# Kernel optimization log

Hardware: AMD Instinct MI355X
Metric: run time of the kernel (lower is better)

Reference implementation:

```python
import jax, jax.numpy as jnp
import numpy as np
from jax import lax

FPS_NUM, K = 2048, 32


def fps_subsample(x, n):
    # x: [B, N, 3] -> [B, n, 3]; farthest point sampling, deterministic start at index 0
    B, N, _ = x.shape
    d0 = jnp.sum((x - x[:, :1]) ** 2, axis=-1)  # [B, N] dist to point 0

    def step(dists, _):
        nxt = jnp.argmax(dists, axis=1)                       # [B]
        p = x[jnp.arange(B), nxt]                             # [B, 3]
        dists = jnp.minimum(dists, jnp.sum((x - p[:, None]) ** 2, axis=-1))
        return dists, nxt

    _, idxs = lax.scan(step, d0, None, length=n - 1)          # [n-1, B]
    idxs = jnp.concatenate([jnp.zeros((1, B), jnp.int32), idxs.astype(jnp.int32)], axis=0).T  # [B, n]
    return x[jnp.arange(B)[:, None], idxs]                    # [B, n, 3]


def knn_idx(x, k):
    # x: [B, C, N] -> [B, N, k] indices of k nearest neighbors in feature space
    xx = jnp.sum(x * x, axis=1)                               # [B, N]
    inner = jnp.einsum('bcn,bcm->bnm', x, x)
    neg_dist = 2.0 * inner - xx[:, :, None] - xx[:, None, :]  # -||xi-xj||^2
    return lax.top_k(neg_dist, k)[1]


def get_graph_feature(x, k):
    # DGCNN edge features: x [B, C, N] -> [B, 2C, N, k]
    B, C, N = x.shape
    idx = knn_idx(x, k)                                       # [B, N, k]
    xt = jnp.transpose(x, (0, 2, 1))                          # [B, N, C]
    nbr = xt[jnp.arange(B)[:, None, None], idx]               # [B, N, k, C]
    ctr = jnp.broadcast_to(xt[:, :, None], nbr.shape)
    feat = jnp.concatenate([nbr - ctr, ctr], axis=-1)         # [B, N, k, 2C]
    return jnp.transpose(feat, (0, 3, 1, 2))


def attention(xq, xk, pos, Wq, bq, Wk, bk, Wv, bv, Wp, bp):
    # positional attention over k neighbors: xq/xk [B, Cin, N, k], pos [B, 3, N] -> [B, dim, N]
    q = jnp.einsum('bcnk,dc->bdnk', xq, Wq) + bq[:, None, None]
    kk = jnp.einsum('bcnk,dc->bdnk', xk, Wk) + bk[:, None, None]
    v = jnp.einsum('bcnk,dc->bdnk', xk, Wv) + bv[:, None, None]
    p = jnp.einsum('bcn,dc->bdn', pos, Wp) + bp[:, None]      # [B, dim, N]
    dim = Wq.shape[0]
    logits = jnp.einsum('bdnk,bdnk->bnk', q, kk) / jnp.sqrt(jnp.float32(dim))
    attn = jax.nn.softmax(logits, axis=-1)                    # [B, N, k]
    return jnp.einsum('bnk,bdnk->bdn', attn, v + p[:, :, :, None])


def _layer_params(key, cin, dim):
    ks = jax.random.split(key, 4)
    s = 1.0 / np.sqrt(cin)
    return (jax.random.normal(ks[0], (dim, cin), jnp.float32) * s,
            jnp.zeros((dim,), jnp.float32),
            jax.random.normal(ks[1], (dim, cin), jnp.float32) * s,
            jnp.zeros((dim,), jnp.float32),
            jax.random.normal(ks[2], (dim, cin), jnp.float32) * s,
            jnp.zeros((dim,), jnp.float32),
            jax.random.normal(ks[3], (dim, 3), jnp.float32) * (1.0 / np.sqrt(3.0)),
            jnp.zeros((dim,), jnp.float32))


def setup_inputs() -> dict:
    key = jax.random.key(0)
    kx, k1, k2, k3 = jax.random.split(key, 4)
    x = jax.random.normal(kx, (8, 16384, 3), jnp.float32)
    out = {'x': x}
    for name, kk_, cin, dim in (('t1', k1, 6, 64), ('t2', k2, 128, 64), ('t3', k3, 128, 128)):
        Wq, bq, Wk, bk, Wv, bv, Wp, bp = _layer_params(kk_, cin, dim)
        out.update({f'{name}_Wq': Wq, f'{name}_bq': bq, f'{name}_Wk': Wk, f'{name}_bk': bk,
                    f'{name}_Wv': Wv, f'{name}_bv': bv, f'{name}_Wp': Wp, f'{name}_bp': bp})
    return out


def reference(x, t1_Wq, t1_bq, t1_Wk, t1_bk, t1_Wv, t1_bv, t1_Wp, t1_bp,
              t2_Wq, t2_bq, t2_Wk, t2_bk, t2_Wv, t2_bv, t2_Wp, t2_bp,
              t3_Wq, t3_bq, t3_Wk, t3_bk, t3_Wv, t3_bv, t3_Wp, t3_bp):
    partial = jnp.transpose(fps_subsample(x, FPS_NUM), (0, 2, 1))       # [B, 3, n]
    g = get_graph_feature(partial, K)                                    # [B, 6, n, k]
    x1 = attention(g, g, partial, t1_Wq, t1_bq, t1_Wk, t1_bk, t1_Wv, t1_bv, t1_Wp, t1_bp)  # [B, 64, n]
    g = get_graph_feature(x1, K)                                         # [B, 128, n, k]
    x2 = attention(g, g, partial, t2_Wq, t2_bq, t2_Wk, t2_bk, t2_Wv, t2_bv, t2_Wp, t2_bp)  # [B, 64, n]
    g = get_graph_feature(x2, K)                                         # [B, 128, n, k]
    x3 = attention(g, g, partial, t3_Wq, t3_bq, t3_Wk, t3_bk, t3_Wv, t3_bv, t3_Wp, t3_bp)  # [B, 128, n]
    feats = jnp.concatenate([x1, x2, x3], axis=1)                        # [B, 256, n]
    return jnp.concatenate([jnp.max(feats, axis=-1), jnp.mean(feats, axis=-1)], axis=1)    # [B, 512]
```

## Files before the change

### kernel.cpp

```cpp
#include <hip/hip_runtime.h>
#include <math.h>

#define NB 8
#define NIN 16384
#define NP 2048
#define KNN 32
#define TOTPTS (NB * NP)

#define NEG_INF (-__builtin_inff())

__device__ __forceinline__ float2 pk_add(float2 a, float2 b) {
  float2 d;
  asm("v_pk_add_f32 %0, %1, %2" : "=v"(d) : "v"(a), "v"(b));
  return d;
}
__device__ __forceinline__ float2 pk_mul(float2 a, float2 b) {
  float2 d;
  asm("v_pk_mul_f32 %0, %1, %2" : "=v"(d) : "v"(a), "v"(b));
  return d;
}

#define DPP_F(old, v, C, RM) \
  __int_as_float(__builtin_amdgcn_update_dpp(__float_as_int(old), __float_as_int(v), C, RM, 0xf, false))
#define DPP_I(old, v, C, RM) \
  __builtin_amdgcn_update_dpp(old, v, C, RM, 0xf, false)

__device__ __forceinline__ float wave_max_f(float v) {
  v = fmaxf(v, DPP_F(NEG_INF, v, 0x111, 0xf));
  v = fmaxf(v, DPP_F(NEG_INF, v, 0x112, 0xf));
  v = fmaxf(v, DPP_F(NEG_INF, v, 0x114, 0xf));
  v = fmaxf(v, DPP_F(NEG_INF, v, 0x118, 0xf));
  v = fmaxf(v, DPP_F(NEG_INF, v, 0x142, 0xa));
  v = fmaxf(v, DPP_F(NEG_INF, v, 0x143, 0xc));
  return v;
}
__device__ __forceinline__ int wave_min_i(int v) {
  v = min(v, DPP_I(0x7fffffff, v, 0x111, 0xf));
  v = min(v, DPP_I(0x7fffffff, v, 0x112, 0xf));
  v = min(v, DPP_I(0x7fffffff, v, 0x114, 0xf));
  v = min(v, DPP_I(0x7fffffff, v, 0x118, 0xf));
  v = min(v, DPP_I(0x7fffffff, v, 0x142, 0xa));
  v = min(v, DPP_I(0x7fffffff, v, 0x143, 0xc));
  return v;
}

template <int CTRL, int RMASK>
__device__ __forceinline__ void dpp_amax_step(float& bv, int& bi) {
  float ov = DPP_F(NEG_INF, bv, CTRL, RMASK);
  int oi = DPP_I(0, bi, CTRL, RMASK);
  if (ov > bv || (ov == bv && oi < bi)) { bv = ov; bi = oi; }
}
__device__ __forceinline__ void wave_amax63(float& bv, int& bi) {
  dpp_amax_step<0x111, 0xf>(bv, bi);
  dpp_amax_step<0x112, 0xf>(bv, bi);
  dpp_amax_step<0x114, 0xf>(bv, bi);
  dpp_amax_step<0x118, 0xf>(bv, bi);
  dpp_amax_step<0x142, 0xa>(bv, bi);
  dpp_amax_step<0x143, 0xc>(bv, bi);
}

__global__ __launch_bounds__(1024) void fps_kernel(const float* __restrict__ x,
                                                   float* __restrict__ partial) {
  const int b = blockIdx.x;
  const int t = threadIdx.x;
  const float* xb = x + (size_t)b * NIN * 3;
  float* pb = partial + (size_t)b * NP * 3;
  __shared__ unsigned long long skey[NP];
  for (int i = t; i < NP; i += 1024) skey[i] = 0ull;

  float2 px[8], py[8], pz[8], dd[8];
#pragma unroll
  for (int j = 0; j < 8; ++j) {
    const int i0 = (2 * j) * 1024 + t, i1 = (2 * j + 1) * 1024 + t;
    px[j] = make_float2(xb[3 * i0], xb[3 * i1]);
    py[j] = make_float2(xb[3 * i0 + 1], xb[3 * i1 + 1]);
    pz[j] = make_float2(xb[3 * i0 + 2], xb[3 * i1 + 2]);
  }
  const float qx0 = xb[0], qy0 = xb[1], qz0 = xb[2];
  if (t == 0) { pb[0] = qx0; pb[1] = qy0; pb[2] = qz0; }

  float bv = NEG_INF;
  int bi = 0;
  {
    const float2 nx2 = make_float2(-qx0, -qx0);
    const float2 ny2 = make_float2(-qy0, -qy0);
    const float2 nz2 = make_float2(-qz0, -qz0);
#pragma unroll
    for (int j = 0; j < 8; ++j) {
      float2 dx = pk_add(px[j], nx2), dy = pk_add(py[j], ny2), dz = pk_add(pz[j], nz2);
      float2 nd = pk_add(pk_add(pk_mul(dx, dx), pk_mul(dy, dy)), pk_mul(dz, dz));
      dd[j] = nd;
      if (nd.x > bv) { bv = nd.x; bi = (2 * j) * 1024 + t; }
      if (nd.y > bv) { bv = nd.y; bi = (2 * j + 1) * 1024 + t; }
    }
  }
  __syncthreads();

  for (int it = 1; it < NP; ++it) {
    const float wm = wave_max_f(bv);
    const float smax = __int_as_float(__builtin_amdgcn_readlane(__float_as_int(wm), 63));
    const int sel = (bv == smax) ? bi : 0x7fffffff;
    const int wi = wave_min_i(sel);
    if ((t & 63) == 63) {
      const unsigned long long key =
          ((unsigned long long)__float_as_uint(smax) << 32) | (unsigned int)(~wi);
      atomicMax(&skey[it], key);
    }
    __syncthreads();
    const unsigned long long gk = skey[it];
    const int gbi = (int)(~(unsigned int)gk);
    const int u = __builtin_amdgcn_readfirstlane(gbi);
    const float nqx = xb[3 * u], nqy = xb[3 * u + 1], nqz = xb[3 * u + 2];
    if (t == 0) { pb[3 * it] = nqx; pb[3 * it + 1] = nqy; pb[3 * it + 2] = nqz; }

    const float2 nx2 = make_float2(-nqx, -nqx);
    const float2 ny2 = make_float2(-nqy, -nqy);
    const float2 nz2 = make_float2(-nqz, -nqz);
    bv = NEG_INF;
    bi = 0;
#pragma unroll
    for (int j = 0; j < 8; ++j) {
      float2 dx = pk_add(px[j], nx2), dy = pk_add(py[j], ny2), dz = pk_add(pz[j], nz2);
      float2 nd = pk_add(pk_add(pk_mul(dx, dx), pk_mul(dy, dy)), pk_mul(dz, dz));
      const float a0 = fminf(dd[j].x, nd.x);
      dd[j].x = a0;
      if (a0 > bv) { bv = a0; bi = (2 * j) * 1024 + t; }
      const float a1 = fminf(dd[j].y, nd.y);
      dd[j].y = a1;
      if (a1 > bv) { bv = a1; bi = (2 * j + 1) * 1024 + t; }
    }
  }
}

__global__ void xx_kernel(const float* __restrict__ F, float* __restrict__ xxg, int C) {
  int i = blockIdx.x * 256 + threadIdx.x;
  if (i >= TOTPTS) return;
  const float* f = F + (size_t)i * C;
  float s = 0.f;
  for (int c = 0; c < C; ++c) s = __fadd_rn(s, __fmul_rn(f[c], f[c]));
  xxg[i] = s;
}

template <int C>
__global__ __launch_bounds__(256) void dist_gemm(const float* __restrict__ F,
                                                 const float* __restrict__ xxg,
                                                 float* __restrict__ D, int bofs) {
  __shared__ float As[64][C + 1];
  __shared__ float Bs[64][C + 1];
  const int b = bofs + blockIdx.z;
  float* Ds = D + (size_t)blockIdx.z * NP * NP;
  const int tid = threadIdx.x;
  const int n0 = blockIdx.y * 64, m0 = blockIdx.x * 64;
  const float* Fb = F + (size_t)b * NP * C;
  const float* xxb = xxg + b * NP;
  for (int t = tid; t < 64 * C; t += 256) {
    int r = t / C, c = t - r * C;
    As[r][c] = Fb[(size_t)(n0 + r) * C + c];
    Bs[r][c] = Fb[(size_t)(m0 + r) * C + c];
  }
  __syncthreads();
  const int tx = tid & 15, ty = tid >> 4;
  float acc[4][4] = {};
  for (int c = 0; c < C; ++c) {
    float a[4], bb[4];
#pragma unroll
    for (int i = 0; i < 4; ++i) a[i] = As[ty * 4 + i][c];
#pragma unroll
    for (int j = 0; j < 4; ++j) bb[j] = Bs[tx * 4 + j][c];
#pragma unroll
    for (int i = 0; i < 4; ++i)
#pragma unroll
      for (int j = 0; j < 4; ++j) acc[i][j] = fmaf(a[i], bb[j], acc[i][j]);
  }
#pragma unroll
  for (int i = 0; i < 4; ++i) {
    int n = n0 + ty * 4 + i;
    float xn = xxb[n];
    float4 o;
    o.x = __fsub_rn(__fsub_rn(2.0f * acc[i][0], xn), xxb[m0 + tx * 4 + 0]);
    o.y = __fsub_rn(__fsub_rn(2.0f * acc[i][1], xn), xxb[m0 + tx * 4 + 1]);
    o.z = __fsub_rn(__fsub_rn(2.0f * acc[i][2], xn), xxb[m0 + tx * 4 + 2]);
    o.w = __fsub_rn(__fsub_rn(2.0f * acc[i][3], xn), xxb[m0 + tx * 4 + 3]);
    *(float4*)&Ds[(size_t)n * NP + m0 + tx * 4] = o;
  }
}

__global__ __launch_bounds__(256) void select_kernel(const float* __restrict__ D,
                                                     int* __restrict__ idxg, int bofs) {
  const int lane = threadIdx.x & 63;
  const int b = bofs + blockIdx.z;
  const int row = blockIdx.x * 4 + (threadIdx.x >> 6);
  const float* Drow = D + (size_t)blockIdx.z * NP * NP + (size_t)row * NP;
  float v[32];
#pragma unroll
  for (int s = 0; s < 32; ++s) v[s] = Drow[s * 64 + lane];
  int* out = idxg + ((size_t)b * NP + row) * KNN;
  for (int t = 0; t < KNN; ++t) {
    float bv = v[0];
    int bs = 0;
#pragma unroll
    for (int s = 1; s < 32; ++s) {
      if (v[s] > bv) { bv = v[s]; bs = s; }
    }
    int bi = bs * 64 + lane;
    wave_amax63(bv, bi);
    const int wbi = __builtin_amdgcn_readlane(bi, 63);
    if (lane == 0) out[t] = wbi;
    const bool own = (lane == (wbi & 63));
    const int cs = wbi >> 6;
#pragma unroll
    for (int s = 0; s < 32; ++s)
      if (own && s == cs) v[s] = NEG_INF;
  }
}

template <int C, int DIM>
__global__ __launch_bounds__(256) void proj_kernel(
    const float* __restrict__ F, const float* __restrict__ pos,
    const float* __restrict__ Wq, const float* __restrict__ bq,
    const float* __restrict__ Wk, const float* __restrict__ bk,
    const float* __restrict__ Wv, const float* __restrict__ bv,
    const float* __restrict__ Wp, const float* __restrict__ bp,
    float* __restrict__ Uq, float* __restrict__ Uk, float* __restrict__ Uv,
    float* __restrict__ Uqc, float* __restrict__ Ukc, float* __restrict__ W6) {
  constexpr int PTS = 16;
  constexpr int GROUPS = 256 / DIM;
  constexpr int PPT = PTS / GROUPS;
  __shared__ float xs[PTS][C];
  __shared__ float ps[PTS][3];
  const int tid = threadIdx.x;
  const int base = blockIdx.x * PTS;
  for (int t = tid; t < PTS * C; t += 256) {
    int r = t / C;
    xs[r][t - r * C] = F[(size_t)(base + r) * C + (t - r * C)];
  }
  for (int t = tid; t < PTS * 3; t += 256) {
    int r = t / 3;
    ps[r][t - r * 3] = pos[(size_t)(base + r) * 3 + (t - r * 3)];
  }
  __syncthreads();
  const int g = tid / DIM;
  const int d = tid - g * DIM;
  float uq[PPT], uqd[PPT], uk[PPT], ukd[PPT], uv[PPT], uvd[PPT];
#pragma unroll
  for (int p = 0; p < PPT; ++p) { uq[p] = uqd[p] = uk[p] = ukd[p] = uv[p] = uvd[p] = 0.f; }
  const float* wqr = Wq + (size_t)d * (2 * C);
  const float* wkr = Wk + (size_t)d * (2 * C);
  const float* wvr = Wv + (size_t)d * (2 * C);
  for (int c = 0; c < C; ++c) {
    const float wq1 = wqr[c], wqd_ = wqr[C + c] - wq1;
    const float wk1 = wkr[c], wkd_ = wkr[C + c] - wk1;
    const float wv1 = wvr[c], wvd_ = wvr[C + c] - wv1;
#pragma unroll
    for (int p = 0; p < PPT; ++p) {
      const float xc = xs[g + p * GROUPS][c];
      uq[p] = fmaf(wq1, xc, uq[p]);
      uqd[p] = fmaf(wqd_, xc, uqd[p]);
      uk[p] = fmaf(wk1, xc, uk[p]);
      ukd[p] = fmaf(wkd_, xc, ukd[p]);
      uv[p] = fmaf(wv1, xc, uv[p]);
      uvd[p] = fmaf(wvd_, xc, uvd[p]);
    }
  }
  const float bqd = bq[d], bkd = bk[d], bvd = bv[d];
  const float wp0 = Wp[d * 3], wp1 = Wp[d * 3 + 1], wp2 = Wp[d * 3 + 2], bpd = bp[d];
#pragma unroll
  for (int p = 0; p < PPT; ++p) {
    const int lp = g + p * GROUPS;
    const size_t o = (size_t)(base + lp) * DIM + d;
    const float pd = wp0 * ps[lp][0] + wp1 * ps[lp][1] + wp2 * ps[lp][2] + bpd;
    Uq[o] = uq[p];
    Uqc[o] = uqd[p] + bqd;
    Uk[o] = uk[p];
    Ukc[o] = ukd[p] + bkd;
    Uv[o] = uv[p];
    W6[o] = uvd[p] + bvd + pd;
  }
}

template <int DIM>
__global__ void prep_kernel(const float* __restrict__ Wq, const float* __restrict__ bq,
                            const float* __restrict__ Wk, const float* __restrict__ bk,
                            const float* __restrict__ Wv, const float* __restrict__ bv,
                            float* __restrict__ Wcat, float* __restrict__ bcat) {
  const int o = blockIdx.x * 256 + threadIdx.x;
  constexpr int ND = 6 * DIM;
  if (o >= ND) return;
  const int blk = o / DIM, d = o % DIM;
  bcat[o] = (blk == 1) ? bq[d] : (blk == 3) ? bk[d] : (blk == 5) ? bv[d] : 0.f;
  const float* W = (blk < 2) ? Wq : (blk < 4) ? Wk : Wv;
  for (int c = 0; c < 64; ++c) {
    const float w1 = W[(size_t)d * 128 + c];
    const float w2 = W[(size_t)d * 128 + 64 + c];
    Wcat[(size_t)c * ND + o] = (blk & 1) ? (w2 - w1) : w1;
  }
}

template <int DIM>
__global__ void pos_kernel(const float* __restrict__ pos, const float* __restrict__ Wp,
                           const float* __restrict__ bp, float* __restrict__ P) {
  const int idx = blockIdx.x * 256 + threadIdx.x;
  const int pt = idx / DIM, d = idx - pt * DIM;
  P[idx] = Wp[d * 3] * pos[pt * 3] + Wp[d * 3 + 1] * pos[pt * 3 + 1] +
           Wp[d * 3 + 2] * pos[pt * 3 + 2] + bp[d];
}

template <int DIM>
__global__ __launch_bounds__(256) void gemm_proj(
    const float* __restrict__ F, const float* __restrict__ Wcat,
    const float* __restrict__ bcat, const float* __restrict__ P,
    float* __restrict__ Uq, float* __restrict__ Uqc, float* __restrict__ Uk,
    float* __restrict__ Ukc, float* __restrict__ Uv, float* __restrict__ W6) {
  constexpr int ND = 6 * DIM;
  __shared__ float As[64][65];
  __shared__ float Bs[64][65];
  const int tid = threadIdx.x;
  const int p0 = blockIdx.x * 64;
  const int n0 = blockIdx.y * 64;
  {
    const int r0 = tid >> 4, c4 = (tid & 15) * 4;
    for (int r = r0; r < 64; r += 16) {
      float4 a = *(const float4*)&F[(size_t)(p0 + r) * 64 + c4];
      As[r][c4] = a.x; As[r][c4 + 1] = a.y; As[r][c4 + 2] = a.z; As[r][c4 + 3] = a.w;
      float4 bb = *(const float4*)&Wcat[(size_t)r * ND + n0 + c4];
      Bs[r][c4] = bb.x; Bs[r][c4 + 1] = bb.y; Bs[r][c4 + 2] = bb.z; Bs[r][c4 + 3] = bb.w;
    }
  }
  __syncthreads();
  const int tx = tid & 15, ty = tid >> 4;
  float acc[4][4] = {};
#pragma unroll 4
  for (int c = 0; c < 64; ++c) {
    float a[4], bb[4];
#pragma unroll
    for (int i = 0; i < 4; ++i) a[i] = As[ty * 4 + i][c];
#pragma unroll
    for (int j = 0; j < 4; ++j) bb[j] = Bs[c][tx * 4 + j];
#pragma unroll
    for (int i = 0; i < 4; ++i)
#pragma unroll
      for (int j = 0; j < 4; ++j) acc[i][j] = fmaf(a[i], bb[j], acc[i][j]);
  }
  const int obuf = n0 / DIM;
  const int oloc = n0 - obuf * DIM;
  float* outp = (obuf == 0) ? Uq : (obuf == 1) ? Uqc : (obuf == 2) ? Uk
              : (obuf == 3) ? Ukc : (obuf == 4) ? Uv : W6;
  const float b0 = bcat[n0 + tx * 4], b1 = bcat[n0 + tx * 4 + 1];
  const float b2 = bcat[n0 + tx * 4 + 2], b3 = bcat[n0 + tx * 4 + 3];
#pragma unroll
  for (int i = 0; i < 4; ++i) {
    const int p = p0 + ty * 4 + i;
    float4 r = make_float4(acc[i][0] + b0, acc[i][1] + b1, acc[i][2] + b2, acc[i][3] + b3);
    if (obuf == 5) {
      float4 pv = *(const float4*)&P[(size_t)p * DIM + oloc + tx * 4];
      r.x += pv.x; r.y += pv.y; r.z += pv.z; r.w += pv.w;
    }
    *(float4*)&outp[(size_t)p * DIM + oloc + tx * 4] = r;
  }
}

template <int DIM>
__global__ __launch_bounds__(256) void attn_kernel(
    const float* __restrict__ Uq, const float* __restrict__ Uk, const float* __restrict__ Uv,
    const float* __restrict__ Uqc, const float* __restrict__ Ukc, const float* __restrict__ W6g,
    const int* __restrict__ idxg, float* __restrict__ outF) {
  const int w = threadIdx.x >> 6, lane = threadIdx.x & 63;
  const int pt = blockIdx.x * 4 + w;
  const int b = pt >> 11;
  __shared__ int sidx[4][KNN];
  __shared__ float sqc[4][DIM], skc[4][DIM], sw6[4][DIM];
  __shared__ float sattn[4][KNN];
  const size_t rowo = (size_t)pt * DIM;
  if (lane < KNN) sidx[w][lane] = idxg[(size_t)pt * KNN + lane];
  for (int d = lane; d < DIM; d += 64) {
    sqc[w][d] = Uqc[rowo + d];
    skc[w][d] = Ukc[rowo + d];
    sw6[w][d] = W6g[rowo + d];
  }
  __syncthreads();
  {
    const int kk = lane & 31;
    const int h = lane >> 5;
    const int ik = sidx[w][kk];
    const float* qr = Uq + (size_t)(b * NP + ik) * DIM;
    const float* kr = Uk + (size_t)(b * NP + ik) * DIM;
    float lg = 0.f;
    const int d0 = h * (DIM / 2), d1 = d0 + DIM / 2;
    for (int d = d0; d < d1; d += 4) {
      float4 qa = *(const float4*)(qr + d);
      float4 ka = *(const float4*)(kr + d);
      float4 qc = *(const float4*)(&sqc[w][d]);
      float4 kc = *(const float4*)(&skc[w][d]);
      lg += (qa.x + qc.x) * (ka.x + kc.x);
      lg += (qa.y + qc.y) * (ka.y + kc.y);
      lg += (qa.z + qc.z) * (ka.z + kc.z);
      lg += (qa.w + qc.w) * (ka.w + kc.w);
    }
    lg += __shfl_xor(lg, 32);
    lg *= (DIM == 64) ? 0.125f : 0.08838834764831845f;
    float m = lg;
#pragma unroll
    for (int off = 16; off; off >>= 1) m = fmaxf(m, __shfl_xor(m, off));
    float e = expf(lg - m);
    float s = e;
#pragma unroll
    for (int off = 16; off; off >>= 1) s += __shfl_xor(s, off);
    if (lane < KNN) sattn[w][lane] = e / s;
  }
  __syncthreads();
  float acc[DIM / 64];
#pragma unroll
  for (int q = 0; q < DIM / 64; ++q) acc[q] = 0.f;
  for (int k = 0; k < KNN; ++k) {
    const int ik = sidx[w][k];
    const float a = sattn[w][k];
    const float* vr = Uv + (size_t)(b * NP + ik) * DIM;
#pragma unroll
    for (int q = 0; q < DIM / 64; ++q) {
      const int d = q * 64 + lane;
      acc[q] = fmaf(a, vr[d] + sw6[w][d], acc[q]);
    }
  }
#pragma unroll
  for (int q = 0; q < DIM / 64; ++q) outF[rowo + q * 64 + lane] = acc[q];
}

__global__ __launch_bounds__(256) void pool_kernel(const float* __restrict__ x1,
                                                   const float* __restrict__ x2,
                                                   const float* __restrict__ x3,
                                                   float* __restrict__ out) {
  const int b = blockIdx.x, c = threadIdx.x;
  const float* src;
  int dim, cl;
  if (c < 64) {
    src = x1 + (size_t)b * NP * 64; dim = 64; cl = c;
  } else if (c < 128) {
    src = x2 + (size_t)b * NP * 64; dim = 64; cl = c - 64;
  } else {
    src = x3 + (size_t)b * NP * 128; dim = 128; cl = c - 128;
  }
  float mx = NEG_INF, sm = 0.f;
#pragma unroll 8
  for (int n = 0; n < NP; ++n) {
    float v = src[(size_t)n * dim + cl];
    mx = fmaxf(mx, v);
    sm += v;
  }
  out[b * 512 + c] = mx;
  out[b * 512 + 256 + c] = sm * (1.0f / 2048.0f);
}

extern "C" void kernel_launch(void* const* d_in, const int* in_sizes, int n_in,
                              void* d_out, int out_size, void* d_ws, size_t ws_size,
                              hipStream_t stream) {
  const float* x = (const float*)d_in[0];
  const float* W[24];
  for (int i = 0; i < 24; ++i) W[i] = (const float*)d_in[1 + i];

  float* ws = (float*)d_ws;
  size_t off = 0;
  float* partial = ws + off; off += (size_t)NB * NP * 3;
  float* xxbuf = ws + off;   off += TOTPTS;
  int* idxb = (int*)(ws + off); off += (size_t)TOTPTS * KNN;
  float* x1 = ws + off; off += (size_t)TOTPTS * 64;
  float* x2 = ws + off; off += (size_t)TOTPTS * 64;
  float* x3 = ws + off; off += (size_t)TOTPTS * 128;
  float* Uq = ws + off;  off += (size_t)TOTPTS * 128;
  float* Uk = ws + off;  off += (size_t)TOTPTS * 128;
  float* Uv = ws + off;  off += (size_t)TOTPTS * 128;
  float* Uqc = ws + off; off += (size_t)TOTPTS * 128;
  float* Ukc = ws + off; off += (size_t)TOTPTS * 128;
  float* W6 = ws + off;  off += (size_t)TOTPTS * 128;
  float* Pbuf = ws + off; off += (size_t)TOTPTS * 128;
  float* Wcat = ws + off; off += (size_t)64 * 768;
  float* bcat = ws + off; off += 768;
  if (ws_size < off * sizeof(float)) return;

  float* Dbig = ws + off;
  const size_t need_big = (off + (size_t)NB * NP * NP) * sizeof(float);
  const bool bigws = (ws_size >= need_big);
  float* D = bigws ? Dbig : Uq;
  const int NZ = bigws ? NB : 1;

  fps_kernel<<<NB, 1024, 0, stream>>>(x, partial);

  xx_kernel<<<TOTPTS / 256, 256, 0, stream>>>(partial, xxbuf, 3);
  for (int b = 0; b < NB; b += NZ) {
    dist_gemm<3><<<dim3(32, 32, NZ), 256, 0, stream>>>(partial, xxbuf, D, b);
    select_kernel<<<dim3(NP / 4, 1, NZ), 256, 0, stream>>>(D, idxb, b);
  }
  proj_kernel<3, 64><<<TOTPTS / 16, 256, 0, stream>>>(
      partial, partial, W[0], W[1], W[2], W[3], W[4], W[5], W[6], W[7],
      Uq, Uk, Uv, Uqc, Ukc, W6);
  attn_kernel<64><<<TOTPTS / 4, 256, 0, stream>>>(Uq, Uk, Uv, Uqc, Ukc, W6, idxb, x1);

  xx_kernel<<<TOTPTS / 256, 256, 0, stream>>>(x1, xxbuf, 64);
  for (int b = 0; b < NB; b += NZ) {
    dist_gemm<64><<<dim3(32, 32, NZ), 256, 0, stream>>>(x1, xxbuf, D, b);
    select_kernel<<<dim3(NP / 4, 1, NZ), 256, 0, stream>>>(D, idxb, b);
  }
  prep_kernel<64><<<2, 256, 0, stream>>>(W[8], W[9], W[10], W[11], W[12], W[13], Wcat, bcat);
  pos_kernel<64><<<TOTPTS * 64 / 256, 256, 0, stream>>>(partial, W[14], W[15], Pbuf);
  gemm_proj<64><<<dim3(TOTPTS / 64, 6), 256, 0, stream>>>(
      x1, Wcat, bcat, Pbuf, Uq, Uqc, Uk, Ukc, Uv, W6);
  attn_kernel<64><<<TOTPTS / 4, 256, 0, stream>>>(Uq, Uk, Uv, Uqc, Ukc, W6, idxb, x2);

  xx_kernel<<<TOTPTS / 256, 256, 0, stream>>>(x2, xxbuf, 64);
  for (int b = 0; b < NB; b += NZ) {
    dist_gemm<64><<<dim3(32, 32, NZ), 256, 0, stream>>>(x2, xxbuf, D, b);
    select_kernel<<<dim3(NP / 4, 1, NZ), 256, 0, stream>>>(D, idxb, b);
  }
  prep_kernel<128><<<3, 256, 0, stream>>>(W[16], W[17], W[18], W[19], W[20], W[21], Wcat, bcat);
  pos_kernel<128><<<TOTPTS * 128 / 256, 256, 0, stream>>>(partial, W[22], W[23], Pbuf);
  gemm_proj<128><<<dim3(TOTPTS / 64, 12), 256, 0, stream>>>(
      x2, Wcat, bcat, Pbuf, Uq, Uqc, Uk, Ukc, Uv, W6);
  attn_kernel<128><<<TOTPTS / 4, 256, 0, stream>>>(Uq, Uk, Uv, Uqc, Ukc, W6, idxb, x3);

  pool_kernel<<<NB, 256, 0, stream>>>(x1, x2, x3, (float*)d_out);
}
```

Before: 4.816 ms.

## Morton-sort input points and skip FPS distance updates for far clusters

A new sort kernel quantizes each batch's points onto a 64^3 grid and bitonic-sorts them by Morton code in shared memory, so each wave's 128-point chunks are spatially compact. The FPS kernel loads points in that order and precomputes a bounding sphere per chunk. Each iteration, it recomputes the chunk's min-distances and argmax only when the new sample could lower some distance in that chunk, judged with a triangle-inequality test against the current max distance. This trades an extra sort launch and per-iteration sphere tests for skipping most of the serial FPS arithmetic, while keeping index tie-breaking via the original ids.

```diff
diff --git a/kernel.cpp b/kernel.cpp
--- a/kernel.cpp
+++ b/kernel.cpp
@@ -8,6 +8,7 @@
 #define TOTPTS (NB * NP)
 
 #define NEG_INF (-__builtin_inff())
+#define POS_INF (__builtin_inff())
 
 __device__ __forceinline__ float2 pk_add(float2 a, float2 b) {
   float2 d;
@@ -34,6 +35,15 @@
   v = fmaxf(v, DPP_F(NEG_INF, v, 0x143, 0xc));
   return v;
 }
+__device__ __forceinline__ float wave_min_f(float v) {
+  v = fminf(v, DPP_F(POS_INF, v, 0x111, 0xf));
+  v = fminf(v, DPP_F(POS_INF, v, 0x112, 0xf));
+  v = fminf(v, DPP_F(POS_INF, v, 0x114, 0xf));
+  v = fminf(v, DPP_F(POS_INF, v, 0x118, 0xf));
+  v = fminf(v, DPP_F(POS_INF, v, 0x142, 0xa));
+  v = fminf(v, DPP_F(POS_INF, v, 0x143, 0xc));
+  return v;
+}
 __device__ __forceinline__ int wave_min_i(int v) {
   v = min(v, DPP_I(0x7fffffff, v, 0x111, 0xf));
   v = min(v, DPP_I(0x7fffffff, v, 0x112, 0xf));
@@ -59,28 +69,142 @@
   dpp_amax_step<0x143, 0xc>(bv, bi);
 }
 
+__device__ __forceinline__ float readlane63f(float v) {
+  return __int_as_float(__builtin_amdgcn_readlane(__float_as_int(v), 63));
+}
+
+__device__ __forceinline__ unsigned f2ord(float f) {
+  unsigned b = __float_as_uint(f);
+  return (b & 0x80000000u) ? ~b : (b | 0x80000000u);
+}
+__device__ __forceinline__ float ord2f(unsigned u) {
+  return __uint_as_float((u & 0x80000000u) ? (u ^ 0x80000000u) : ~u);
+}
+__device__ __forceinline__ unsigned spread3(unsigned v) {
+  return (v & 1u) | ((v & 2u) << 2) | ((v & 4u) << 4) | ((v & 8u) << 6) |
+         ((v & 16u) << 8) | ((v & 32u) << 10);
+}
+
+__global__ __launch_bounds__(1024) void sort_kernel(const float* __restrict__ x,
+                                                    unsigned* __restrict__ ord) {
+  const int b = blockIdx.x, t = threadIdx.x;
+  const float* xb = x + (size_t)b * NIN * 3;
+  __shared__ unsigned keys[NIN];
+  __shared__ unsigned smn[3], smx[3];
+  if (t < 3) { smn[t] = 0xFFFFFFFFu; smx[t] = 0u; }
+  __syncthreads();
+  float cx[16], cy[16], cz[16];
+  float mnx = POS_INF, mny = POS_INF, mnz = POS_INF;
+  float mxx = NEG_INF, mxy = NEG_INF, mxz = NEG_INF;
+#pragma unroll
+  for (int s = 0; s < 16; ++s) {
+    const int i = s * 1024 + t;
+    cx[s] = xb[3 * i]; cy[s] = xb[3 * i + 1]; cz[s] = xb[3 * i + 2];
+    mnx = fminf(mnx, cx[s]); mxx = fmaxf(mxx, cx[s]);
+    mny = fminf(mny, cy[s]); mxy = fmaxf(mxy, cy[s]);
+    mnz = fminf(mnz, cz[s]); mxz = fmaxf(mxz, cz[s]);
+  }
+  mnx = wave_min_f(mnx); mxx = wave_max_f(mxx);
+  mny = wave_min_f(mny); mxy = wave_max_f(mxy);
+  mnz = wave_min_f(mnz); mxz = wave_max_f(mxz);
+  if ((t & 63) == 63) {
+    atomicMin(&smn[0], f2ord(mnx)); atomicMax(&smx[0], f2ord(mxx));
+    atomicMin(&smn[1], f2ord(mny)); atomicMax(&smx[1], f2ord(mxy));
+    atomicMin(&smn[2], f2ord(mnz)); atomicMax(&smx[2], f2ord(mxz));
+  }
+  __syncthreads();
+  const float bx = ord2f(smn[0]), by = ord2f(smn[1]), bz = ord2f(smn[2]);
+  const float fx = 63.9f / fmaxf(ord2f(smx[0]) - bx, 1e-30f);
+  const float fy = 63.9f / fmaxf(ord2f(smx[1]) - by, 1e-30f);
+  const float fz = 63.9f / fmaxf(ord2f(smx[2]) - bz, 1e-30f);
+#pragma unroll
+  for (int s = 0; s < 16; ++s) {
+    const int i = s * 1024 + t;
+    const unsigned a0 = min(63u, (unsigned)(int)fmaxf((cx[s] - bx) * fx, 0.f));
+    const unsigned a1 = min(63u, (unsigned)(int)fmaxf((cy[s] - by) * fy, 0.f));
+    const unsigned a2 = min(63u, (unsigned)(int)fmaxf((cz[s] - bz) * fz, 0.f));
+    const unsigned code = spread3(a0) | (spread3(a1) << 1) | (spread3(a2) << 2);
+    keys[i] = (code << 14) | (unsigned)i;
+  }
+  __syncthreads();
+  for (unsigned k = 2; k <= (unsigned)NIN; k <<= 1) {
+    for (unsigned j = k >> 1; j; j >>= 1) {
+#pragma unroll
+      for (int s = 0; s < 8; ++s) {
+        const unsigned idx = (unsigned)t + (unsigned)s * 1024u;
+        const unsigned e = ((idx & ~(j - 1u)) << 1) | (idx & (j - 1u));
+        const unsigned p = e | j;
+        const unsigned a = keys[e], c = keys[p];
+        if ((a > c) == ((e & k) == 0u)) { keys[e] = c; keys[p] = a; }
+      }
+      __syncthreads();
+    }
+  }
+#pragma unroll
+  for (int s = 0; s < 16; ++s) {
+    const int i = s * 1024 + t;
+    ord[(size_t)b * NIN + i] = keys[i] & 0x3FFFu;
+  }
+}
+
+#define FPS_UPD(j)                                                            \
+  {                                                                           \
+    float2 dx = pk_add(px[j], nx2), dy = pk_add(py[j], ny2), dz = pk_add(pz[j], nz2); \
+    float2 nd = pk_add(pk_add(pk_mul(dx, dx), pk_mul(dy, dy)), pk_mul(dz, dz));        \
+    dd[j].x = fminf(dd[j].x, nd.x);                                           \
+    dd[j].y = fminf(dd[j].y, nd.y);                                           \
+  }
+
 __global__ __launch_bounds__(1024) void fps_kernel(const float* __restrict__ x,
+                                                   const unsigned* __restrict__ ord,
                                                    float* __restrict__ partial) {
   const int b = blockIdx.x;
   const int t = threadIdx.x;
+  const int w = t >> 6, l = t & 63;
   const float* xb = x + (size_t)b * NIN * 3;
   float* pb = partial + (size_t)b * NP * 3;
   __shared__ unsigned long long skey[NP];
   for (int i = t; i < NP; i += 1024) skey[i] = 0ull;
 
   float2 px[8], py[8], pz[8], dd[8];
+  int id0[8], id1[8];
+  const unsigned* ob = ord + (size_t)b * NIN;
 #pragma unroll
   for (int j = 0; j < 8; ++j) {
-    const int i0 = (2 * j) * 1024 + t, i1 = (2 * j + 1) * 1024 + t;
-    px[j] = make_float2(xb[3 * i0], xb[3 * i1]);
-    py[j] = make_float2(xb[3 * i0 + 1], xb[3 * i1 + 1]);
-    pz[j] = make_float2(xb[3 * i0 + 2], xb[3 * i1 + 2]);
-  }
+    const int p0 = ((w * 8 + j) << 7) + l * 2;
+    const int g0 = (int)ob[p0], g1 = (int)ob[p0 + 1];
+    id0[j] = g0; id1[j] = g1;
+    px[j] = make_float2(xb[3 * g0], xb[3 * g1]);
+    py[j] = make_float2(xb[3 * g0 + 1], xb[3 * g1 + 1]);
+    pz[j] = make_float2(xb[3 * g0 + 2], xb[3 * g1 + 2]);
+  }
+
+  float ccx = 0.f, ccy = 0.f, ccz = 0.f, ccr = 0.f;
+#pragma unroll
+  for (int j = 0; j < 8; ++j) {
+    float mnx = wave_min_f(fminf(px[j].x, px[j].y));
+    float mxx = wave_max_f(fmaxf(px[j].x, px[j].y));
+    float mny = wave_min_f(fminf(py[j].x, py[j].y));
+    float mxy = wave_max_f(fmaxf(py[j].x, py[j].y));
+    float mnz = wave_min_f(fminf(pz[j].x, pz[j].y));
+    float mxz = wave_max_f(fmaxf(pz[j].x, pz[j].y));
+    const float cx = 0.5f * (readlane63f(mnx) + readlane63f(mxx));
+    const float cy = 0.5f * (readlane63f(mny) + readlane63f(mxy));
+    const float cz = 0.5f * (readlane63f(mnz) + readlane63f(mxz));
+    float d0x = px[j].x - cx, d0y = py[j].x - cy, d0z = pz[j].x - cz;
+    float d1x = px[j].y - cx, d1y = py[j].y - cy, d1z = pz[j].y - cz;
+    float d2 = fmaxf(d0x * d0x + d0y * d0y + d0z * d0z,
+                     d1x * d1x + d1y * d1y + d1z * d1z);
+    d2 = wave_max_f(d2);
+    const float r = sqrtf(readlane63f(d2)) * 1.00002f;
+    if (l == j) { ccx = cx; ccy = cy; ccz = cz; ccr = r; }
+  }
+
   const float qx0 = xb[0], qy0 = xb[1], qz0 = xb[2];
   if (t == 0) { pb[0] = qx0; pb[1] = qy0; pb[2] = qz0; }
 
   float bv = NEG_INF;
-  int bi = 0;
+  int bi = 0x7fffffff;
   {
     const float2 nx2 = make_float2(-qx0, -qx0);
     const float2 ny2 = make_float2(-qy0, -qy0);
@@ -90,44 +214,53 @@
       float2 dx = pk_add(px[j], nx2), dy = pk_add(py[j], ny2), dz = pk_add(pz[j], nz2);
       float2 nd = pk_add(pk_add(pk_mul(dx, dx), pk_mul(dy, dy)), pk_mul(dz, dz));
       dd[j] = nd;
-      if (nd.x > bv) { bv = nd.x; bi = (2 * j) * 1024 + t; }
-      if (nd.y > bv) { bv = nd.y; bi = (2 * j + 1) * 1024 + t; }
+      if (nd.x > bv || (nd.x == bv && id0[j] < bi)) { bv = nd.x; bi = id0[j]; }
+      if (nd.y > bv || (nd.y == bv && id1[j] < bi)) { bv = nd.y; bi = id1[j]; }
     }
   }
   __syncthreads();
 
   for (int it = 1; it < NP; ++it) {
     const float wm = wave_max_f(bv);
-    const float smax = __int_as_float(__builtin_amdgcn_readlane(__float_as_int(wm), 63));
-    const int sel = (bv == smax) ? bi : 0x7fffffff;
+    const float smaxw = readlane63f(wm);
+    const int sel = (bv == smaxw) ? bi : 0x7fffffff;
     const int wi = wave_min_i(sel);
-    if ((t & 63) == 63) {
+    if (l == 63) {
       const unsigned long long key =
-          ((unsigned long long)__float_as_uint(smax) << 32) | (unsigned int)(~wi);
+          ((unsigned long long)__float_as_uint(smaxw) << 32) | (unsigned)(~wi);
       atomicMax(&skey[it], key);
     }
     __syncthreads();
     const unsigned long long gk = skey[it];
-    const int gbi = (int)(~(unsigned int)gk);
-    const int u = __builtin_amdgcn_readfirstlane(gbi);
+    const float smax = __uint_as_float((unsigned)(gk >> 32));
+    const int u = __builtin_amdgcn_readfirstlane((int)(~(unsigned)gk));
     const float nqx = xb[3 * u], nqy = xb[3 * u + 1], nqz = xb[3 * u + 2];
     if (t == 0) { pb[3 * it] = nqx; pb[3 * it + 1] = nqy; pb[3 * it + 2] = nqz; }
 
-    const float2 nx2 = make_float2(-nqx, -nqx);
-    const float2 ny2 = make_float2(-nqy, -nqy);
-    const float2 nz2 = make_float2(-nqz, -nqz);
-    bv = NEG_INF;
-    bi = 0;
-#pragma unroll
-    for (int j = 0; j < 8; ++j) {
-      float2 dx = pk_add(px[j], nx2), dy = pk_add(py[j], ny2), dz = pk_add(pz[j], nz2);
-      float2 nd = pk_add(pk_add(pk_mul(dx, dx), pk_mul(dy, dy)), pk_mul(dz, dz));
-      const float a0 = fminf(dd[j].x, nd.x);
-      dd[j].x = a0;
-      if (a0 > bv) { bv = a0; bi = (2 * j) * 1024 + t; }
-      const float a1 = fminf(dd[j].y, nd.y);
-      dd[j].y = a1;
-      if (a1 > bv) { bv = a1; bi = (2 * j + 1) * 1024 + t; }
+    const float rho = sqrtf(smax) * 1.00002f;
+    const float cdx = ccx - nqx, cdy = ccy - nqy, cdz = ccz - nqz;
+    const float dq = sqrtf(cdx * cdx + cdy * cdy + cdz * cdz);
+    const bool upd = (l < 8) && (dq * 0.99998f < ccr + rho);
+    const unsigned m8 = (unsigned)__ballot(upd) & 255u;
+    if (m8) {
+      const float2 nx2 = make_float2(-nqx, -nqx);
+      const float2 ny2 = make_float2(-nqy, -nqy);
+      const float2 nz2 = make_float2(-nqz, -nqz);
+      if (m8 & 1u) FPS_UPD(0)
+      if (m8 & 2u) FPS_UPD(1)
+      if (m8 & 4u) FPS_UPD(2)
+      if (m8 & 8u) FPS_UPD(3)
+      if (m8 & 16u) FPS_UPD(4)
+      if (m8 & 32u) FPS_UPD(5)
+      if (m8 & 64u) FPS_UPD(6)
+      if (m8 & 128u) FPS_UPD(7)
+      bv = NEG_INF;
+      bi = 0x7fffffff;
+#pragma unroll
+      for (int j = 0; j < 8; ++j) {
+        if (dd[j].x > bv || (dd[j].x == bv && id0[j] < bi)) { bv = dd[j].x; bi = id0[j]; }
+        if (dd[j].y > bv || (dd[j].y == bv && id1[j] < bi)) { bv = dd[j].y; bi = id1[j]; }
+      }
     }
   }
 }
@@ -462,6 +595,7 @@
   float* partial = ws + off; off += (size_t)NB * NP * 3;
   float* xxbuf = ws + off;   off += TOTPTS;
   int* idxb = (int*)(ws + off); off += (size_t)TOTPTS * KNN;
+  unsigned* ordb = (unsigned*)(ws + off); off += (size_t)NB * NIN;
   float* x1 = ws + off; off += (size_t)TOTPTS * 64;
   float* x2 = ws + off; off += (size_t)TOTPTS * 64;
   float* x3 = ws + off; off += (size_t)TOTPTS * 128;
@@ -482,7 +616,8 @@
   float* D = bigws ? Dbig : Uq;
   const int NZ = bigws ? NB : 1;
 
-  fps_kernel<<<NB, 1024, 0, stream>>>(x, partial);
+  sort_kernel<<<NB, 1024, 0, stream>>>(x, ordb);
+  fps_kernel<<<NB, 1024, 0, stream>>>(x, ordb, partial);
 
   xx_kernel<<<TOTPTS / 256, 256, 0, stream>>>(partial, xxbuf, 3);
   for (int b = 0; b < NB; b += NZ) {
```

Result: slower. 5.240 ms (+8.8%).

## Fuse 3-D distance, norm and top-k selection into one kNN kernel

Applied to the files above, without the earlier changes.

For the first kNN stage (C=3), a single kernel now loads the batch's points and squared norms into shared memory, computes each row's distances in registers, and runs top-k selection there. This replaces the xx_kernel, dist_gemm and select_kernel sequence and removes the round trip of the full NxN distance matrix through global memory. Separately, the wave argmax in select_kernel now uses a float wave-max followed by an int wave-min on the index, instead of paired value/index DPP steps with branches. The new kernel recomputes per-block shared loads of all 2048 points, and its fused-multiply-add distance arithmetic may round differently from the GEMM path, which could change tie order.

```diff
diff --git a/kernel.cpp b/kernel.cpp
--- a/kernel.cpp
+++ b/kernel.cpp
@@ -8,6 +8,7 @@
 #define TOTPTS (NB * NP)
 
 #define NEG_INF (-__builtin_inff())
+#define POS_INF (__builtin_inff())
 
 __device__ __forceinline__ float2 pk_add(float2 a, float2 b) {
   float2 d;
@@ -44,19 +45,8 @@
   return v;
 }
 
-template <int CTRL, int RMASK>
-__device__ __forceinline__ void dpp_amax_step(float& bv, int& bi) {
-  float ov = DPP_F(NEG_INF, bv, CTRL, RMASK);
-  int oi = DPP_I(0, bi, CTRL, RMASK);
-  if (ov > bv || (ov == bv && oi < bi)) { bv = ov; bi = oi; }
-}
-__device__ __forceinline__ void wave_amax63(float& bv, int& bi) {
-  dpp_amax_step<0x111, 0xf>(bv, bi);
-  dpp_amax_step<0x112, 0xf>(bv, bi);
-  dpp_amax_step<0x114, 0xf>(bv, bi);
-  dpp_amax_step<0x118, 0xf>(bv, bi);
-  dpp_amax_step<0x142, 0xa>(bv, bi);
-  dpp_amax_step<0x143, 0xc>(bv, bi);
+__device__ __forceinline__ float readlane63f(float v) {
+  return __int_as_float(__builtin_amdgcn_readlane(__float_as_int(v), 63));
 }
 
 __global__ __launch_bounds__(1024) void fps_kernel(const float* __restrict__ x,
@@ -98,7 +88,7 @@
 
   for (int it = 1; it < NP; ++it) {
     const float wm = wave_max_f(bv);
-    const float smax = __int_as_float(__builtin_amdgcn_readlane(__float_as_int(wm), 63));
+    const float smax = readlane63f(wm);
     const int sel = (bv == smax) ? bi : 0x7fffffff;
     const int wi = wave_min_i(sel);
     if ((t & 63) == 63) {
@@ -139,6 +129,55 @@
   float s = 0.f;
   for (int c = 0; c < C; ++c) s = __fadd_rn(s, __fmul_rn(f[c], f[c]));
   xxg[i] = s;
+}
+
+__global__ __launch_bounds__(1024) void knn3_kernel(const float* __restrict__ F,
+                                                    int* __restrict__ idxg) {
+  const int b = blockIdx.z;
+  const int t = threadIdx.x;
+  const int w = t >> 6, lane = t & 63;
+  __shared__ float spx[NP], spy[NP], spz[NP], sxx[NP];
+  const float* Fb = F + (size_t)b * NP * 3;
+  for (int i = t; i < NP; i += 1024) {
+    const float a0 = Fb[3 * i], a1 = Fb[3 * i + 1], a2 = Fb[3 * i + 2];
+    spx[i] = a0; spy[i] = a1; spz[i] = a2;
+    float s = __fadd_rn(0.f, __fmul_rn(a0, a0));
+    s = __fadd_rn(s, __fmul_rn(a1, a1));
+    s = __fadd_rn(s, __fmul_rn(a2, a2));
+    sxx[i] = s;
+  }
+  __syncthreads();
+  const int row = blockIdx.x * 16 + w;
+  const float a0 = spx[row], a1 = spy[row], a2 = spz[row];
+  const float xn = sxx[row];
+  float v[32];
+#pragma unroll
+  for (int s = 0; s < 32; ++s) {
+    const int m = s * 64 + lane;
+    float acc = fmaf(a0, spx[m], 0.f);
+    acc = fmaf(a1, spy[m], acc);
+    acc = fmaf(a2, spz[m], acc);
+    v[s] = __fsub_rn(__fsub_rn(2.0f * acc, xn), sxx[m]);
+  }
+  int* out = idxg + ((size_t)b * NP + row) * KNN;
+  for (int tt = 0; tt < KNN; ++tt) {
+    float bv = v[0];
+    int bs = 0;
+#pragma unroll
+    for (int s = 1; s < 32; ++s) {
+      if (v[s] > bv) { bv = v[s]; bs = s; }
+    }
+    int bi = bs * 64 + lane;
+    const float vmax = readlane63f(wave_max_f(bv));
+    const int sel = (bv == vmax) ? bi : 0x7fffffff;
+    const int wbi = __builtin_amdgcn_readlane(wave_min_i(sel), 63);
+    if (lane == 0) out[tt] = wbi;
+    const bool own = (lane == (wbi & 63));
+    const int cs = wbi >> 6;
+#pragma unroll
+    for (int s = 0; s < 32; ++s)
+      if (own && s == cs) v[s] = NEG_INF;
+  }
 }
 
 template <int C>
@@ -203,8 +242,9 @@
       if (v[s] > bv) { bv = v[s]; bs = s; }
     }
     int bi = bs * 64 + lane;
-    wave_amax63(bv, bi);
-    const int wbi = __builtin_amdgcn_readlane(bi, 63);
+    const float vmax = readlane63f(wave_max_f(bv));
+    const int sel = (bv == vmax) ? bi : 0x7fffffff;
+    const int wbi = __builtin_amdgcn_readlane(wave_min_i(sel), 63);
     if (lane == 0) out[t] = wbi;
     const bool own = (lane == (wbi & 63));
     const int cs = wbi >> 6;
@@ -484,11 +524,7 @@
 
   fps_kernel<<<NB, 1024, 0, stream>>>(x, partial);
 
-  xx_kernel<<<TOTPTS / 256, 256, 0, stream>>>(partial, xxbuf, 3);
-  for (int b = 0; b < NB; b += NZ) {
-    dist_gemm<3><<<dim3(32, 32, NZ), 256, 0, stream>>>(partial, xxbuf, D, b);
-    select_kernel<<<dim3(NP / 4, 1, NZ), 256, 0, stream>>>(D, idxb, b);
-  }
+  knn3_kernel<<<dim3(NP / 16, 1, NB), 1024, 0, stream>>>(partial, idxb);
   proj_kernel<3, 64><<<TOTPTS / 16, 256, 0, stream>>>(
       partial, partial, W[0], W[1], W[2], W[3], W[4], W[5], W[6], W[7],
       Uq, Uk, Uv, Uqc, Ukc, W6);
```

After: 4.719 ms. 1.02x faster.
